# Performance work log

Measured on AMD Instinct MI355X. Metric: run time of the kernel, lower is better.

## Reference

```python
import jax, jax.numpy as jnp
import numpy as np

NUM_NODES = 100000
NUM_RELATIONS = 16
HIDDEN = 64
NUM_LAYERS = 3
NUM_EDGES = 1600000


def setup_inputs() -> dict:
    key = jax.random.key(0)
    ks = jax.random.split(key, 6)
    edge_index = jax.random.randint(ks[0], (2, NUM_EDGES), 0, NUM_NODES, dtype=jnp.int64 if jax.config.jax_enable_x64 else jnp.int32)
    edge_type = jax.random.randint(ks[1], (NUM_EDGES,), 0, NUM_RELATIONS, dtype=edge_index.dtype)
    scale = 1.0 / np.sqrt(HIDDEN)
    node_emb = jax.random.normal(ks[2], (NUM_NODES, HIDDEN), dtype=jnp.float32) * scale
    # Per-layer relation weights [L, R, d, h], root weights [L, d, h], bias [L, h]
    W = jax.random.normal(ks[3], (NUM_LAYERS, NUM_RELATIONS, HIDDEN, HIDDEN), dtype=jnp.float32) * scale
    W_root = jax.random.normal(ks[4], (NUM_LAYERS, HIDDEN, HIDDEN), dtype=jnp.float32) * scale
    bias = jnp.zeros((NUM_LAYERS, HIDDEN), dtype=jnp.float32)
    return {"edge_index": edge_index, "edge_type": edge_type,
            "node_emb": node_emb, "W": W, "W_root": W_root, "bias": bias}


def _rgcn_layer(x, src, dst, et, Wr, Wroot, b):
    # PyG RGCNConv: out_i = W_root x_i + b + sum_r (1/|N_r(i)|) sum_{j in N_r(i)} W_r x_j
    N, d = x.shape
    R = Wr.shape[0]
    # Transform all nodes by every relation weight: [R, N, h] (dense grouped GEMM)
    xW = jnp.einsum('nd,rdh->rnh', x, Wr)
    m = xW[et, src]                      # [E, h] per-edge messages (gather)
    seg = dst * R + et                   # joint (dst, relation) segment id
    counts = jax.ops.segment_sum(jnp.ones((m.shape[0],), dtype=x.dtype), seg, num_segments=N * R)
    norm = 1.0 / jnp.maximum(counts, 1.0)
    m = m * norm[seg][:, None]           # per-relation mean normalization
    agg = jax.ops.segment_sum(m, dst, num_segments=N)  # scatter-add over dst
    return agg + x @ Wroot + b


def reference(edge_index, edge_type, node_emb, W, W_root, bias):
    src, dst = edge_index[0], edge_index[1]
    x = node_emb  # note: Embedding.max_norm only applies on index lookups; .weight used raw here
    n_layers = W.shape[0]
    for i in range(n_layers):
        x = _rgcn_layer(x, src, dst, edge_type, W[i], W_root[i], bias[i])
        if i < n_layers - 1:
            x = jax.nn.relu(x)
    return x
```

## Files before the change

### kernel.cpp

```cpp
#include <hip/hip_runtime.h>


#define HID   64
#define NREL  16
#define KD    1088
#define NPB   16
#define NPW   2
#define LSTR  1096

#define NBKT  1024
#define BSH   7
#define FB    2048
#define CAPB  4096
#define CHA   8192

typedef __attribute__((ext_vector_type(8))) short bf16x8;
typedef __attribute__((ext_vector_type(4))) float f32x4;
typedef unsigned short us16;
typedef unsigned int u32;

__device__ __forceinline__ float b2f(us16 u) {
    union { u32 i; float f; } c; c.i = ((u32)u) << 16; return c.f;
}
__device__ __forceinline__ us16 f2b(float f) {
    union { float f; u32 i; } c; c.f = f;
    u32 x = c.i;
    return (us16)((x + 0x7FFFu + ((x >> 16) & 1u)) >> 16);
}


__global__ __launch_bounds__(256) void bucket_count(const int* __restrict__ ei,
                                                    int* __restrict__ counts_b, int E) {
    __shared__ int h[NBKT];
    const int t = threadIdx.x;
    for (int i = t; i < NBKT; i += 256) h[i] = 0;
    __syncthreads();
    const int* dstp = ei + E;
    int start = blockIdx.x * CHA, end = min(start + CHA, E);
    for (int e4 = start + t * 4; e4 < end; e4 += 1024) {
        if (e4 + 3 < end) {
            int4 d = *(const int4*)(dstp + e4);
            atomicAdd(&h[d.x >> BSH], 1);
            atomicAdd(&h[d.y >> BSH], 1);
            atomicAdd(&h[d.z >> BSH], 1);
            atomicAdd(&h[d.w >> BSH], 1);
        } else {
            for (int e = e4; e < end; ++e) atomicAdd(&h[dstp[e] >> BSH], 1);
        }
    }
    __syncthreads();
    for (int i = t; i < NBKT; i += 256) {
        int v = h[i];
        if (v) atomicAdd(&counts_b[i], v);
    }
}

__global__ __launch_bounds__(NBKT) void scan_buckets(const int* __restrict__ counts_b,
                                                     int* __restrict__ bucket_base,
                                                     int* __restrict__ cursor_b,
                                                     int* __restrict__ row_ptr,
                                                     int N, int E) {
    __shared__ int s[NBKT];
    int t = threadIdx.x;
    int v = counts_b[t];
    s[t] = v; __syncthreads();
    for (int off = 1; off < NBKT; off <<= 1) {
        int tv = (t >= off) ? s[t - off] : 0;
        __syncthreads();
        s[t] += tv;
        __syncthreads();
    }
    int ex = s[t] - v;
    bucket_base[t] = ex;
    cursor_b[t] = ex;
    if (t == NBKT - 1) bucket_base[NBKT] = ex + v;
    if (t == 0) row_ptr[N] = E;
}

__global__ __launch_bounds__(256) void bucket_place(const int* __restrict__ ei,
                                                    const int* __restrict__ et,
                                                    int* __restrict__ cursor_b,
                                                    u32* __restrict__ packed, int E) {
    __shared__ int cnt[NBKT];
    __shared__ int bse[NBKT];
    const int t = threadIdx.x;
    for (int i = t; i < NBKT; i += 256) cnt[i] = 0;
    __syncthreads();
    const int* dstp = ei + E;
    int start = blockIdx.x * CHA, end = min(start + CHA, E);
    for (int e4 = start + t * 4; e4 < end; e4 += 1024) {
        if (e4 + 3 < end) {
            int4 d = *(const int4*)(dstp + e4);
            atomicAdd(&cnt[d.x >> BSH], 1);
            atomicAdd(&cnt[d.y >> BSH], 1);
            atomicAdd(&cnt[d.z >> BSH], 1);
            atomicAdd(&cnt[d.w >> BSH], 1);
        } else {
            for (int e = e4; e < end; ++e) atomicAdd(&cnt[dstp[e] >> BSH], 1);
        }
    }
    __syncthreads();
    for (int i = t; i < NBKT; i += 256) {
        int v = cnt[i];
        bse[i] = v ? atomicAdd(&cursor_b[i], v) : 0;
        cnt[i] = 0;
    }
    __syncthreads();
    #define PLACE1(sv, dv, tv)                                            \
        { int b_ = (dv) >> BSH;                                           \
          int r_ = atomicAdd(&cnt[b_], 1);                                \
          packed[bse[b_] + r_] = (u32)(sv) | ((u32)(tv) << 17)            \
                               | ((u32)((dv) & 127) << 21); }
    for (int e4 = start + t * 4; e4 < end; e4 += 1024) {
        if (e4 + 3 < end) {
            int4 sv = *(const int4*)(ei + e4);
            int4 dv = *(const int4*)(dstp + e4);
            int4 tv = *(const int4*)(et + e4);
            PLACE1(sv.x, dv.x, tv.x);
            PLACE1(sv.y, dv.y, tv.y);
            PLACE1(sv.z, dv.z, tv.z);
            PLACE1(sv.w, dv.w, tv.w);
        } else {
            for (int e = e4; e < end; ++e) PLACE1(ei[e], dstp[e], et[e]);
        }
    }
    #undef PLACE1
}

__global__ __launch_bounds__(256) void bucket_sort(const u32* __restrict__ packed,
                                                   const int* __restrict__ bucket_base,
                                                   u32* __restrict__ md,
                                                   int* __restrict__ row_ptr, int N) {
    __shared__ int hist[FB];
    __shared__ int ss[256];
    __shared__ u32 outb[CAPB];
    const int b = blockIdx.x, t = threadIdx.x;
    const int base = bucket_base[b];
    const int cnt = bucket_base[b + 1] - base;

    for (int i = t; i < FB; i += 256) hist[i] = 0;
    __syncthreads();
    for (int i = t; i < cnt; i += 256) {
        u32 p = packed[base + i];
        int f = (int)(((p >> 21) & 127u) * 16u + ((p >> 17) & 15u));
        atomicAdd(&hist[f], 1);
    }
    __syncthreads();
    int loc[8], s = 0;
    #pragma unroll
    for (int j = 0; j < 8; ++j) { loc[j] = hist[t * 8 + j]; s += loc[j]; }
    ss[t] = s; __syncthreads();
    for (int off = 1; off < 256; off <<= 1) {
        int tv = (t >= off) ? ss[t - off] : 0;
        __syncthreads();
        ss[t] += tv;
        __syncthreads();
    }
    int run = ss[t] - s;
    #pragma unroll
    for (int j = 0; j < 8; ++j) { hist[t * 8 + j] = run; run += loc[j]; }
    __syncthreads();
    if (t < 128) {
        int node = b * 128 + t;
        if (node < N) row_ptr[node] = base + hist[t * 16];
    }
    __syncthreads();
    for (int i = t; i < cnt; i += 256) {
        u32 p = packed[base + i];
        int f = (int)(((p >> 21) & 127u) * 16u + ((p >> 17) & 15u));
        int pos = atomicAdd(&hist[f], 1);
        u32 v = (p & 0x1FFFFu) | (((p >> 17) & 15u) << 20);
        if (pos < CAPB) outb[pos] = v;
        else            md[base + pos] = v;
    }
    __syncthreads();
    for (int i = t; i < cnt && i < CAPB; i += 256)
        md[base + i] = outb[i];
}

__global__ void convx_kernel(const float* __restrict__ x, us16* __restrict__ xb, int n4) {
    int i = blockIdx.x * 256 + threadIdx.x;
    if (i < n4) {
        float4 v = ((const float4*)x)[i];
        us16* o = xb + i * 4;
        o[0] = f2b(v.x); o[1] = f2b(v.y); o[2] = f2b(v.z); o[3] = f2b(v.w);
    }
}

__global__ void convw_kernel(const float* __restrict__ W, const float* __restrict__ Wroot,
                             us16* __restrict__ WcatT, int total, int L) {
    int i = blockIdx.x * 256 + threadIdx.x;
    if (i < total) {
        int l = i / (HID * KD);
        int rem = i % (HID * KD);
        int h = rem / KD, k = rem % KD;
        float v;
        if (k < NREL * HID) {
            int r = k >> 6, d = k & 63;
            v = W[(((size_t)l * NREL + r) * HID + d) * HID + h];
        } else {
            int d = k - NREL * HID;
            v = Wroot[((size_t)l * HID + d) * HID + h];
        }
        WcatT[i] = f2b(v);
    }
}


__device__ __forceinline__ void issue16(u32 p_l, int c, int wcnt,
                                        const us16* __restrict__ x_in, int lane,
                                        int* pe, us16* hv) {
    int last = wcnt - 1; if (last < 0) last = 0;
    #pragma unroll
    for (int j = 0; j < 16; ++j) {
        int idx = c + j; if (idx > last) idx = last;
        pe[j] = __builtin_amdgcn_readlane((int)p_l, idx);
        hv[j] = x_in[((u32)pe[j] & 0xFFFFFu) * HID + lane];
    }
}

__device__ __forceinline__ void consume16(const int* pe, const us16* hv, int c, int wcnt,
                                          us16* Hrow, int lane,
                                          float& acc, int& runlen, int& prev, u32& mask) {
    #pragma unroll
    for (int j = 0; j < 16; ++j) {
        if (c + j < wcnt) {
            int r = (int)(((u32)pe[j]) >> 20);
            if (r != prev) {
                if (prev >= 0) {
                    Hrow[(prev << 6) + lane] =
                        f2b(acc * __builtin_amdgcn_rcpf((float)runlen));
                    mask |= 1u << prev;
                }
                prev = r; acc = 0.f; runlen = 0;
            }
            acc += b2f(hv[j]); ++runlen;
        }
    }
}

__device__ __forceinline__ void proc_node(int node, int start, int cnt, u32 plq,
                                          const us16* __restrict__ x_in,
                                          const u32* __restrict__ md,
                                          us16* Hrow, us16 xrq, int lane, int N,
                                          int* pe, us16* hv) {
    if (node >= N) return;
    Hrow[NREL * HID + lane] = xrq;
    float acc = 0.f;
    int runlen = 0, prev = -1;
    u32 mask = 0;

    int wcnt = cnt < 64 ? cnt : 64;
    consume16(pe, hv, 0, wcnt, Hrow, lane, acc, runlen, prev, mask);
    for (int c = 16; c < wcnt; c += 16) {
        issue16(plq, c, wcnt, x_in, lane, pe, hv);
        consume16(pe, hv, c, wcnt, Hrow, lane, acc, runlen, prev, mask);
    }
    for (int w0s = 64; w0s < cnt; w0s += 64) {
        int wc = cnt - w0s; if (wc > 64) wc = 64;
        u32 p2 = (lane < wc) ? md[start + w0s + lane] : 0;
        for (int c = 0; c < wc; c += 16) {
            issue16(p2, c, wc, x_in, lane, pe, hv);
            consume16(pe, hv, c, wc, Hrow, lane, acc, runlen, prev, mask);
        }
    }
    if (prev >= 0) {
        Hrow[(prev << 6) + lane] = f2b(acc * __builtin_amdgcn_rcpf((float)runlen));
        mask |= 1u << prev;
    }
    #pragma unroll
    for (int r = 0; r < NREL; ++r)
        if (!(mask & (1u << r))) Hrow[(r << 6) + lane] = 0;
}

__global__ __launch_bounds__(512, 8) void layer_kernel(
        const us16* __restrict__ x_in,
        const int*  __restrict__ row_ptr,
        const u32*  __restrict__ md,
        const us16* __restrict__ WcatT,
        const float* __restrict__ bias,
        us16* __restrict__ x_out,
        float* __restrict__ out_f32,
        int flags, int N)
{
    __shared__ us16 H[NPB * LSTR];
    __shared__ float P[NPB * HID];
    const int tid = threadIdx.x, wave = tid >> 6, lane = tid & 63;
    const int node0 = blockIdx.x * NPB;
    const int nodeq = node0 + wave * NPW;

    int rp[NPW + 1];
    #pragma unroll
    for (int i = 0; i <= NPW; ++i)
        rp[i] = __builtin_amdgcn_readfirstlane(row_ptr[min(nodeq + i, N)]);

    u32 pl[NPW]; us16 xr[NPW];
    #pragma unroll
    for (int q = 0; q < NPW; ++q) {
        int cnt = rp[q + 1] - rp[q];
        pl[q] = (lane < cnt) ? md[rp[q] + lane] : 0;
        xr[q] = (nodeq + q < N) ? x_in[(nodeq + q) * HID + lane] : (us16)0;
    }

    int peA[16], peB[16]; us16 hvA[16], hvB[16];
    int w0 = rp[1] - rp[0]; if (w0 > 64) w0 = 64;
    int w1 = rp[2] - rp[1]; if (w1 > 64) w1 = 64;
    issue16(pl[0], 0, w0, x_in, lane, peA, hvA);
    issue16(pl[1], 0, w1, x_in, lane, peB, hvB);

    proc_node(nodeq + 0, rp[0], rp[1] - rp[0], pl[0], x_in, md,
              H + (wave * NPW + 0) * LSTR, xr[0], lane, N, peA, hvA);
    proc_node(nodeq + 1, rp[1], rp[2] - rp[1], pl[1], x_in, md,
              H + (wave * NPW + 1) * LSTR, xr[1], lane, N, peB, hvB);
    __syncthreads();

    {
        const int n16 = lane & 15, quad = lane >> 4;
        const int kw = wave >> 2;
        const int wv = wave & 3;
        f32x4 acc = {0.f, 0.f, 0.f, 0.f};
        const us16* Abase = H + n16 * LSTR + quad * 8 + kw * (KD / 2);
        const us16* Bbase = WcatT + (size_t)(wv * 16 + n16) * KD + quad * 8 + kw * (KD / 2);
        #pragma unroll
        for (int ks = 0; ks < KD / 64; ++ks) {
            bf16x8 af = *(const bf16x8*)(Abase + ks * 32);
            bf16x8 bf = *(const bf16x8*)(Bbase + ks * 32);
            acc = __builtin_amdgcn_mfma_f32_16x16x32_bf16(af, bf, acc, 0, 0, 0);
        }

        int col = wv * 16 + n16;
        if (kw) {
            #pragma unroll
            for (int ri = 0; ri < 4; ++ri)
                P[(quad * 4 + ri) * HID + col] = acc[ri];
        }
        __syncthreads();
        if (!kw) {
            float bv = bias[col];
            #pragma unroll
            for (int ri = 0; ri < 4; ++ri) {
                int nl = quad * 4 + ri, node = node0 + nl;
                if (node < N) {
                    float v = acc[ri] + P[nl * HID + col] + bv;
                    if (flags & 1) v = fmaxf(v, 0.f);
                    if (flags & 2) out_f32[node * HID + col] = v;
                    else           x_out [node * HID + col] = f2b(v);
                }
            }
        }
    }
}


extern "C" void kernel_launch(void* const* d_in, const int* in_sizes, int n_in,
                              void* d_out, int out_size, void* d_ws, size_t ws_size,
                              hipStream_t stream) {
    const int*   edge_index = (const int*)  d_in[0];
    const int*   edge_type  = (const int*)  d_in[1];
    const float* node_emb   = (const float*)d_in[2];
    const float* W          = (const float*)d_in[3];
    const float* Wroot      = (const float*)d_in[4];
    const float* bias       = (const float*)d_in[5];
    float* out = (float*)d_out;

    const int E = in_sizes[1];
    const int N = in_sizes[2] / HID;
    const int L = in_sizes[5] / HID;

    char* p = (char*)d_ws;
    size_t off = 0;
    auto carve = [&](size_t bytes) {
        void* q = p + off;
        off = (off + bytes + 255) & ~(size_t)255;
        return q;
    };
    int*   counts_b    = (int*)  carve((size_t)NBKT * 4);
    int*   bucket_base = (int*)  carve((size_t)(NBKT + 1) * 4);
    int*   cursor_b    = (int*)  carve((size_t)NBKT * 4);
    int*   row_ptr     = (int*)  carve((size_t)(N + 1) * 4);
    u32*   packed      = (u32*)  carve((size_t)E * 4);
    u32*   md          = (u32*)  carve((size_t)E * 4);
    us16*  xb0         = (us16*) carve((size_t)N * HID * 2);
    us16*  xb1         = (us16*) carve((size_t)N * HID * 2);
    us16*  WcatT       = (us16*) carve((size_t)L * HID * KD * 2);
    (void)ws_size; (void)n_in; (void)out_size;

    hipMemsetAsync(counts_b, 0, (size_t)NBKT * 4, stream);

    const int nblkA = (E + CHA - 1) / CHA;
    bucket_count<<<nblkA, 256, 0, stream>>>(edge_index, counts_b, E);
    scan_buckets<<<1, NBKT, 0, stream>>>(counts_b, bucket_base, cursor_b, row_ptr, N, E);
    bucket_place<<<nblkA, 256, 0, stream>>>(edge_index, edge_type, cursor_b, packed, E);
    bucket_sort<<<(N + 127) / 128, 256, 0, stream>>>(packed, bucket_base, md, row_ptr, N);

    convx_kernel<<<(N * HID / 4 + 255) / 256, 256, 0, stream>>>(node_emb, xb0, N * HID / 4);
    int wtot = L * HID * KD;
    convw_kernel<<<(wtot + 255) / 256, 256, 0, stream>>>(W, Wroot, WcatT, wtot, L);

    int gl = (N + NPB - 1) / NPB;
    us16* xin = xb0;
    us16* xother = xb1;
    for (int l = 0; l < L; ++l) {
        int last = (l == L - 1);
        int flags = (last ? 2 : 1);
        layer_kernel<<<gl, 512, 0, stream>>>(
            xin, row_ptr, md,
            WcatT + (size_t)l * HID * KD, bias + (size_t)l * HID,
            last ? nullptr : xother, last ? out : nullptr,
            flags, N);
        us16* t = xin; xin = xother; xother = t;
    }
}
```

Baseline: 539.5 us.

## Merge per-wave node pair into one triple-buffered gather pipeline

Each wave now treats its two nodes' edge lists as one contiguous range, offsetting relation ids for the second node. Gathers are issued three 16-edge batches ahead in a rotating triple buffer fenced by sched_barriers. Empty relation slots are zeroed up front instead of tracked with a mask. The aim is more loads in flight per wave to hide gather latency, paid for with extra registers, so occupancy is lowered to 6 in launch bounds and the LDS stride is changed.

```diff
diff --git a/kernel.cpp b/kernel.cpp
--- a/kernel.cpp
+++ b/kernel.cpp
@@ -5,8 +5,7 @@
 #define NREL  16
 #define KD    1088
 #define NPB   16
-#define NPW   2
-#define LSTR  1096
+#define LSTR  1104
 
 #define NBKT  1024
 #define BSH   7
@@ -207,31 +206,36 @@
 }
 
 
-__device__ __forceinline__ void issue16(u32 p_l, int c, int wcnt,
-                                        const us16* __restrict__ x_in, int lane,
-                                        int* pe, us16* hv) {
-    int last = wcnt - 1; if (last < 0) last = 0;
+__device__ __forceinline__ void issue16b(u32 pl, int c, int cnt,
+                                         const us16* __restrict__ x_in, int lane,
+                                         int* pe, us16* hv) {
+    int w0 = c & ~63;
+    int wl = cnt - w0; if (wl > 64) wl = 64; --wl;
+    int cb = c & 63;
     #pragma unroll
     for (int j = 0; j < 16; ++j) {
-        int idx = c + j; if (idx > last) idx = last;
-        pe[j] = __builtin_amdgcn_readlane((int)p_l, idx);
+        int rl = cb + j; if (rl > wl) rl = wl;
+        pe[j] = __builtin_amdgcn_readlane((int)pl, rl);
         hv[j] = x_in[((u32)pe[j] & 0xFFFFFu) * HID + lane];
     }
 }
 
-__device__ __forceinline__ void consume16(const int* pe, const us16* hv, int c, int wcnt,
-                                          us16* Hrow, int lane,
-                                          float& acc, int& runlen, int& prev, u32& mask) {
+__device__ __forceinline__ void flush_seg(us16* Hbase, int prev, float acc,
+                                          int runlen, int lane) {
+    int off = ((prev >> 4) * LSTR) + ((prev & 15) << 6);
+    Hbase[off + lane] = f2b(acc * __builtin_amdgcn_rcpf((float)runlen));
+}
+
+__device__ __forceinline__ void consume16b(const int* pe, const us16* hv, int c, int cnt,
+                                           int b1, us16* Hbase, int lane,
+                                           float& acc, int& runlen, int& prev) {
     #pragma unroll
     for (int j = 0; j < 16; ++j) {
-        if (c + j < wcnt) {
-            int r = (int)(((u32)pe[j]) >> 20);
+        int idx = c + j;
+        if (idx < cnt) {
+            int r = (int)(((u32)pe[j]) >> 20) + ((idx >= b1) ? 16 : 0);
             if (r != prev) {
-                if (prev >= 0) {
-                    Hrow[(prev << 6) + lane] =
-                        f2b(acc * __builtin_amdgcn_rcpf((float)runlen));
-                    mask |= 1u << prev;
-                }
+                if (prev >= 0) flush_seg(Hbase, prev, acc, runlen, lane);
                 prev = r; acc = 0.f; runlen = 0;
             }
             acc += b2f(hv[j]); ++runlen;
@@ -239,41 +243,7 @@
     }
 }
 
-__device__ __forceinline__ void proc_node(int node, int start, int cnt, u32 plq,
-                                          const us16* __restrict__ x_in,
-                                          const u32* __restrict__ md,
-                                          us16* Hrow, us16 xrq, int lane, int N,
-                                          int* pe, us16* hv) {
-    if (node >= N) return;
-    Hrow[NREL * HID + lane] = xrq;
-    float acc = 0.f;
-    int runlen = 0, prev = -1;
-    u32 mask = 0;
-
-    int wcnt = cnt < 64 ? cnt : 64;
-    consume16(pe, hv, 0, wcnt, Hrow, lane, acc, runlen, prev, mask);
-    for (int c = 16; c < wcnt; c += 16) {
-        issue16(plq, c, wcnt, x_in, lane, pe, hv);
-        consume16(pe, hv, c, wcnt, Hrow, lane, acc, runlen, prev, mask);
-    }
-    for (int w0s = 64; w0s < cnt; w0s += 64) {
-        int wc = cnt - w0s; if (wc > 64) wc = 64;
-        u32 p2 = (lane < wc) ? md[start + w0s + lane] : 0;
-        for (int c = 0; c < wc; c += 16) {
-            issue16(p2, c, wc, x_in, lane, pe, hv);
-            consume16(pe, hv, c, wc, Hrow, lane, acc, runlen, prev, mask);
-        }
-    }
-    if (prev >= 0) {
-        Hrow[(prev << 6) + lane] = f2b(acc * __builtin_amdgcn_rcpf((float)runlen));
-        mask |= 1u << prev;
-    }
-    #pragma unroll
-    for (int r = 0; r < NREL; ++r)
-        if (!(mask & (1u << r))) Hrow[(r << 6) + lane] = 0;
-}
-
-__global__ __launch_bounds__(512, 8) void layer_kernel(
+__global__ __launch_bounds__(512, 6) void layer_kernel(
         const us16* __restrict__ x_in,
         const int*  __restrict__ row_ptr,
         const u32*  __restrict__ md,
@@ -287,31 +257,66 @@
     __shared__ float P[NPB * HID];
     const int tid = threadIdx.x, wave = tid >> 6, lane = tid & 63;
     const int node0 = blockIdx.x * NPB;
-    const int nodeq = node0 + wave * NPW;
-
-    int rp[NPW + 1];
-    #pragma unroll
-    for (int i = 0; i <= NPW; ++i)
-        rp[i] = __builtin_amdgcn_readfirstlane(row_ptr[min(nodeq + i, N)]);
-
-    u32 pl[NPW]; us16 xr[NPW];
-    #pragma unroll
-    for (int q = 0; q < NPW; ++q) {
-        int cnt = rp[q + 1] - rp[q];
-        pl[q] = (lane < cnt) ? md[rp[q] + lane] : 0;
-        xr[q] = (nodeq + q < N) ? x_in[(nodeq + q) * HID + lane] : (us16)0;
-    }
-
-    int peA[16], peB[16]; us16 hvA[16], hvB[16];
-    int w0 = rp[1] - rp[0]; if (w0 > 64) w0 = 64;
-    int w1 = rp[2] - rp[1]; if (w1 > 64) w1 = 64;
-    issue16(pl[0], 0, w0, x_in, lane, peA, hvA);
-    issue16(pl[1], 0, w1, x_in, lane, peB, hvB);
-
-    proc_node(nodeq + 0, rp[0], rp[1] - rp[0], pl[0], x_in, md,
-              H + (wave * NPW + 0) * LSTR, xr[0], lane, N, peA, hvA);
-    proc_node(nodeq + 1, rp[1], rp[2] - rp[1], pl[1], x_in, md,
-              H + (wave * NPW + 1) * LSTR, xr[1], lane, N, peB, hvB);
+
+    {
+        const int nodeq = node0 + wave * 2;
+        const int rp0 = __builtin_amdgcn_readfirstlane(row_ptr[min(nodeq,     N)]);
+        const int rp1 = __builtin_amdgcn_readfirstlane(row_ptr[min(nodeq + 1, N)]);
+        const int rp2 = __builtin_amdgcn_readfirstlane(row_ptr[min(nodeq + 2, N)]);
+        us16* Hbase = H + wave * 2 * LSTR;
+
+        {
+            u32* hz0 = (u32*)Hbase;
+            u32* hz1 = (u32*)(Hbase + LSTR);
+            #pragma unroll
+            for (int i = 0; i < 8; ++i) { hz0[i * 64 + lane] = 0; hz1[i * 64 + lane] = 0; }
+        }
+        if (nodeq < N)     Hbase[NREL * HID + lane]        = x_in[(size_t)nodeq * HID + lane];
+        if (nodeq + 1 < N) Hbase[LSTR + NREL * HID + lane] = x_in[(size_t)(nodeq + 1) * HID + lane];
+
+        const int cnt = rp2 - rp0;
+        const int b1  = rp1 - rp0;
+        float acc = 0.f; int runlen = 0, prev = -1;
+
+        if (cnt > 0) {
+            int wc0 = cnt < 64 ? cnt : 64;
+            u32 pl = (lane < wc0) ? md[rp0 + lane] : 0u;
+            int peA[16], peB[16], peC[16];
+            us16 hvA[16], hvB[16], hvC[16];
+            issue16b(pl, 0, cnt, x_in, lane, peA, hvA);
+            if (cnt > 16) issue16b(pl, 16, cnt, x_in, lane, peB, hvB);
+            if (cnt > 32) issue16b(pl, 32, cnt, x_in, lane, peC, hvC);
+            const int nb = (cnt + 15) >> 4;
+            int b = 0;
+            for (;;) {
+                __builtin_amdgcn_sched_barrier(0);
+                consume16b(peA, hvA, b << 4, cnt, b1, Hbase, lane, acc, runlen, prev);
+                if (++b >= nb) break;
+                { int c3 = (b + 2) << 4;
+                  if (c3 < cnt) {
+                      if ((c3 & 63) == 0) { int wc = cnt - c3; if (wc > 64) wc = 64;
+                                            pl = (lane < wc) ? md[rp0 + c3 + lane] : 0u; }
+                      issue16b(pl, c3, cnt, x_in, lane, peA, hvA); } }
+                __builtin_amdgcn_sched_barrier(0);
+                consume16b(peB, hvB, b << 4, cnt, b1, Hbase, lane, acc, runlen, prev);
+                if (++b >= nb) break;
+                { int c3 = (b + 2) << 4;
+                  if (c3 < cnt) {
+                      if ((c3 & 63) == 0) { int wc = cnt - c3; if (wc > 64) wc = 64;
+                                            pl = (lane < wc) ? md[rp0 + c3 + lane] : 0u; }
+                      issue16b(pl, c3, cnt, x_in, lane, peB, hvB); } }
+                __builtin_amdgcn_sched_barrier(0);
+                consume16b(peC, hvC, b << 4, cnt, b1, Hbase, lane, acc, runlen, prev);
+                if (++b >= nb) break;
+                { int c3 = (b + 2) << 4;
+                  if (c3 < cnt) {
+                      if ((c3 & 63) == 0) { int wc = cnt - c3; if (wc > 64) wc = 64;
+                                            pl = (lane < wc) ? md[rp0 + c3 + lane] : 0u; }
+                      issue16b(pl, c3, cnt, x_in, lane, peC, hvC); } }
+            }
+            if (prev >= 0) flush_seg(Hbase, prev, acc, runlen, lane);
+        }
+    }
     __syncthreads();
 
     {
```

New measurement: 587.4 us. +8.9%, slower.
